# Performance work log

Hardware: AMD Instinct MI355X
Metric: run time of the kernel (lower is better)

## Reference

```python
import jax, jax.numpy as jnp
import numpy as np

B, S, T, D, V = 512, 128, 128, 512, 128  # batch, enc len, dec steps (=longest_smi), dim_model, output_size


def setup_inputs() -> dict:
    key = jax.random.key(0)
    ks = jax.random.split(key, 17)
    sc = 0.05
    return {
        "e_all": jax.random.normal(ks[0], (B, S, D), jnp.float32),
        "e_h": jax.random.normal(ks[1], (1, B, D), jnp.float32),
        "e_c": jax.random.normal(ks[2], (1, B, D), jnp.float32),
        "target": jax.random.randint(ks[3], (B, T), 0, T),
        # params (Linear weights stored [in, out], y = x @ W + b)
        "E": jax.random.normal(ks[4], (T, D), jnp.float32) * sc,        # Embedding(longest_smi, D)
        "Wa": jax.random.normal(ks[5], (D, D), jnp.float32) * sc,
        "ba": jnp.zeros((D,), jnp.float32),
        "Ua": jax.random.normal(ks[6], (D, D), jnp.float32) * sc,
        "bu": jnp.zeros((D,), jnp.float32),
        "Va": jax.random.normal(ks[7], (D, 1), jnp.float32) * sc,
        "bv": jnp.zeros((1,), jnp.float32),
        "W_ih": jax.random.normal(ks[8], (2 * D, 4 * D), jnp.float32) * sc,
        "b_ih": jnp.zeros((4 * D,), jnp.float32),
        "W_hh": jax.random.normal(ks[9], (D, 4 * D), jnp.float32) * sc,
        "b_hh": jnp.zeros((4 * D,), jnp.float32),
        "W_out": jax.random.normal(ks[10], (D, V), jnp.float32) * sc,
        "b_out": jnp.zeros((V,), jnp.float32),
    }


def reference(e_all, e_h, e_c, target, E, Wa, ba, Ua, bu, Va, bv,
              W_ih, b_ih, W_hh, b_hh, W_out, b_out):
    Bb = e_all.shape[0]
    # teacher forcing: step 0 input is token 0 (SOS), then target[:, :-1]
    idx = jnp.concatenate([jnp.zeros((Bb, 1), target.dtype), target[:, :-1]], axis=1)  # [B,T]
    emb_all = E[idx]                       # [B,T,D] (dropout is identity in eval)
    keys_proj = e_all @ Ua + bu            # Ua(keys), loop-invariant  [B,S,D]
    h0, c0 = e_h[0], e_c[0]                # [B,D]

    def step(carry, emb):
        h, c = carry
        q = (h + c) @ Wa + ba                                   # [B,D]  Wa(query)
        s = jnp.tanh(q[:, None, :] + keys_proj) @ Va + bv       # [B,S,1]
        w = jax.nn.softmax(s[..., 0], axis=-1)                  # [B,S]
        ctx = jnp.einsum('bs,bsd->bd', w, e_all)                # [B,D]
        x = jnp.concatenate([emb, ctx], axis=-1)                # [B,2D]
        g = x @ W_ih + b_ih + h @ W_hh + b_hh                   # [B,4D], torch gate order i,f,g,o
        i_, f_, g_, o_ = jnp.split(g, 4, axis=-1)
        c2 = jax.nn.sigmoid(f_) * c + jax.nn.sigmoid(i_) * jnp.tanh(g_)
        h2 = jax.nn.sigmoid(o_) * jnp.tanh(c2)
        out = h2 @ W_out + b_out                                # [B,V]
        return (h2, c2), (out, w)

    _, (outs, attns) = jax.lax.scan(step, (h0, c0), jnp.swapaxes(emb_all, 0, 1))
    outputs = jax.nn.log_softmax(jnp.swapaxes(outs, 0, 1), axis=-1)  # [B,T,V]
    cross_attn = jnp.swapaxes(attns, 0, 1)                           # [B,T,S]
    return outputs, cross_attn
```

## Files before the change

kernel.cpp:

```cpp
#include <hip/hip_runtime.h>

#define B_ 512
#define S_ 128
#define T_ 128
#define D_ 512
#define V_ 128
#define LDW 72

typedef __attribute__((ext_vector_type(8))) short s16x8;
typedef __attribute__((ext_vector_type(4))) short s16x4;
typedef __attribute__((ext_vector_type(4))) float f32x4;

__device__ __forceinline__ float b2f(unsigned short h) {
    union { unsigned int u; float f; } x; x.u = ((unsigned int)h) << 16; return x.f;
}
__device__ __forceinline__ unsigned short f2b(float f) {
    union { float f; unsigned int u; } x; x.f = f;
    unsigned int u = x.u; u += 0x7FFFu + ((u >> 16) & 1u);
    return (unsigned short)(u >> 16);
}
#if __has_builtin(__builtin_amdgcn_rcpf)
__device__ __forceinline__ float rcp_f(float x) { return __builtin_amdgcn_rcpf(x); }
#else
__device__ __forceinline__ float rcp_f(float x) { return 1.0f / x; }
#endif
__device__ __forceinline__ float sigm(float x) { return rcp_f(1.0f + __expf(-x)); }
__device__ __forceinline__ float tanh_fast(float x) {
    float e = __expf(2.0f * fabsf(x));
    float r = 1.0f - 2.0f * rcp_f(e + 1.0f);
    return copysignf(r, x);
}

#if __has_builtin(__builtin_amdgcn_cvt_f32_fp8)
__device__ __forceinline__ f32x4 fp8x4_dec(unsigned w) {
    f32x4 r;
    r[0] = __builtin_amdgcn_cvt_f32_fp8(w, 0);
    r[1] = __builtin_amdgcn_cvt_f32_fp8(w, 1);
    r[2] = __builtin_amdgcn_cvt_f32_fp8(w, 2);
    r[3] = __builtin_amdgcn_cvt_f32_fp8(w, 3);
    return r;
}
#else
__device__ __forceinline__ float fp8_dec_sw(unsigned w, int j) {
    unsigned char v = (w >> (8 * j)) & 0xFF;
    unsigned s = v >> 7, e = (v >> 3) & 0xF, m = v & 7;
    float r = (e == 0) ? ldexpf((float)m, -9) : ldexpf((float)(8 + m), (int)e - 10);
    return s ? -r : r;
}
__device__ __forceinline__ f32x4 fp8x4_dec(unsigned w) {
    f32x4 r;
    r[0] = fp8_dec_sw(w, 0); r[1] = fp8_dec_sw(w, 1);
    r[2] = fp8_dec_sw(w, 2); r[3] = fp8_dec_sw(w, 3);
    return r;
}
#endif

#if __has_builtin(__builtin_amdgcn_cvt_pk_fp8_f32)
__device__ __forceinline__ unsigned pk_fp8(float a, float b, float c, float d) {
    int r = 0;
    r = __builtin_amdgcn_cvt_pk_fp8_f32(a, b, r, false);
    r = __builtin_amdgcn_cvt_pk_fp8_f32(c, d, r, true);
    return (unsigned)r;
}
#else
__device__ __forceinline__ unsigned char f32_to_fp8_sw(float x) {
    unsigned s = x < 0.f ? 0x80u : 0u; float a = fabsf(x);
    if (a != a) return (unsigned char)(s | 0x7F);
    if (a >= 448.f) return (unsigned char)(s | 0x7E);
    if (a < 0.001953125f) { int m = (int)rintf(a * 512.0f); return (unsigned char)(s | (m > 7 ? 0x08 : m)); }
    int e; float fr = frexpf(a, &e);
    int m = (int)rintf(fr * 16.0f - 8.0f);
    int ee = e - 1 + 7;
    if (m == 8) { m = 0; ee += 1; }
    if (ee <= 0) { int mm = (int)rintf(a * 512.f); return (unsigned char)(s | (mm > 7 ? 0x08 : mm)); }
    if (ee >= 16) return (unsigned char)(s | 0x7E);
    return (unsigned char)(s | (ee << 3) | m);
}
__device__ __forceinline__ unsigned pk_fp8(float a, float b, float c, float d) {
    return (unsigned)f32_to_fp8_sw(a) | ((unsigned)f32_to_fp8_sw(b) << 8)
         | ((unsigned)f32_to_fp8_sw(c) << 16) | ((unsigned)f32_to_fp8_sw(d) << 24);
}
#endif

struct P {
    const int* target;
    const float* E; const float* bv; const float* ba; const float* bout;
    const short* vab;
    const unsigned char* ea8; const unsigned char* kp8;
    const short* WaT; const short* WehT; const short* WctxT; const short* WoutT;
    const float* bcat;
    short* qbf; short* xeh; short* ctxb; short* gpb;
    short* hcbf; short* h2bf; float* cst;
    float* out_logits; float* out_attn;
};

struct AttnS { float scp[4][64]; float wbuf[S_]; float cpart[4][D_]; };
struct OutS  { short As[64][LDW]; short Bs[128][LDW]; };
struct PG2   { short As[128][LDW]; short Bs[64][LDW]; };
struct GateS { short As[64][LDW]; short Bs[64][LDW]; float gt[64][65]; };
union SharedA { AttnS a; OutS o; };
union SharedC { OutS o; PG2 g; };

__device__ __forceinline__ void attn_phase(const P& p, AttnS& sh, int b, int step)
{
    const int t = threadIdx.x, lane = t & 63, wave = t >> 6;
    {
        const int sg = wave & 1, dh = wave >> 1;
        const int s = sg * 64 + lane;
        const unsigned char* kb = p.kp8 + (size_t)b * (S_ * D_);
        const short* qv = p.qbf + (size_t)b * D_;
        float acc = 0.f;
        #pragma unroll 4
        for (int i = 0; i < 16; ++i) {
            int g = dh * 16 + i;
            uint4 kw = *(const uint4*)(kb + ((size_t)g * 128 + s) * 16);
            const short* qg = qv + g * 16;
            const short* vg = p.vab + g * 16;
            s16x8 q0 = *(const s16x8*)(qg), q1 = *(const s16x8*)(qg + 8);
            s16x8 v0 = *(const s16x8*)(vg), v1 = *(const s16x8*)(vg + 8);
            f32x4 ka = fp8x4_dec(kw.x), kb4 = fp8x4_dec(kw.y);
            f32x4 kc = fp8x4_dec(kw.z), kd = fp8x4_dec(kw.w);
            #pragma unroll
            for (int j = 0; j < 4; ++j) {
                acc += tanh_fast(b2f((unsigned short)q0[j])     + ka[j])  * b2f((unsigned short)v0[j]);
                acc += tanh_fast(b2f((unsigned short)q0[4 + j]) + kb4[j]) * b2f((unsigned short)v0[4 + j]);
                acc += tanh_fast(b2f((unsigned short)q1[j])     + kc[j])  * b2f((unsigned short)v1[j]);
                acc += tanh_fast(b2f((unsigned short)q1[4 + j]) + kd[j])  * b2f((unsigned short)v1[4 + j]);
            }
        }
        sh.scp[wave][lane] = acc;
    }
    __syncthreads();
    if (wave == 0) {
        const float bvv = p.bv[0];
        float v0 = sh.scp[0][lane] + sh.scp[2][lane] + bvv;
        float v1 = sh.scp[1][lane] + sh.scp[3][lane] + bvv;
        float m = fmaxf(v0, v1);
        #pragma unroll
        for (int o = 32; o >= 1; o >>= 1) m = fmaxf(m, __shfl_xor(m, o));
        float e0 = __expf(v0 - m), e1 = __expf(v1 - m);
        float su = e0 + e1;
        #pragma unroll
        for (int o = 32; o >= 1; o >>= 1) su += __shfl_xor(su, o);
        float inv = rcp_f(su);
        float w0 = e0 * inv, w1 = e1 * inv;
        sh.wbuf[lane] = w0; sh.wbuf[lane + 64] = w1;
        float* ao = p.out_attn + ((size_t)b * T_ + step) * S_;
        ao[lane] = w0; ao[lane + 64] = w1;
    }
    __syncthreads();
    {
        const int d0 = lane * 8;
        f32x4 aA = {0.f,0.f,0.f,0.f}, aB = {0.f,0.f,0.f,0.f};
        const unsigned char* eb = p.ea8 + (size_t)b * S_ * D_ + d0;
        #pragma unroll 4
        for (int i = 0; i < 32; ++i) {
            int s = wave * 32 + i;
            float wv = sh.wbuf[s];
            uint2 ev = *(const uint2*)(eb + (size_t)s * D_);
            f32x4 ex = fp8x4_dec(ev.x), ey = fp8x4_dec(ev.y);
            #pragma unroll
            for (int j = 0; j < 4; ++j) aA[j] += wv * ex[j];
            #pragma unroll
            for (int j = 0; j < 4; ++j) aB[j] += wv * ey[j];
        }
        *(f32x4*)&sh.cpart[wave][d0]     = aA;
        *(f32x4*)&sh.cpart[wave][d0 + 4] = aB;
    }
    __syncthreads();
    {
        int dd = t * 2;
        float v0 = sh.cpart[0][dd]   + sh.cpart[1][dd]   + sh.cpart[2][dd]   + sh.cpart[3][dd];
        float v1 = sh.cpart[0][dd+1] + sh.cpart[1][dd+1] + sh.cpart[2][dd+1] + sh.cpart[3][dd+1];
        short2 o2; o2.x = (short)f2b(v0); o2.y = (short)f2b(v1);
        *(short2*)(p.ctxb + (size_t)b * D_ + dd) = o2;
    }
}

__device__ __forceinline__ void pgate_phase(const P& p, PG2& sh, int bid2)
{
    const int t = threadIdx.x, lane = t & 63, wave = t >> 6;
    const int lrow = lane & 15, kq = lane >> 4;
    const int m0 = (bid2 >> 5) * 128, n0 = (bid2 & 31) * 64;
    const int K = 1024;
    f32x4 acc[2][4] = {};
    for (int k0 = 0; k0 < K; k0 += 64) {
        s16x8 va[4], vb[2];
        #pragma unroll
        for (int r = 0; r < 4; ++r) {
            int idx = r * 256 + t, row = idx >> 3, seg = idx & 7;
            va[r] = *(const s16x8*)(p.xeh + (size_t)(m0 + row) * K + k0 + seg * 8);
        }
        #pragma unroll
        for (int r = 0; r < 2; ++r) {
            int idx = r * 256 + t, row = idx >> 3, seg = idx & 7;
            vb[r] = *(const s16x8*)(p.WehT + (size_t)(n0 + row) * K + k0 + seg * 8);
        }
        __syncthreads();
        #pragma unroll
        for (int r = 0; r < 4; ++r) {
            int idx = r * 256 + t, row = idx >> 3, seg = idx & 7;
            *(s16x8*)(&sh.As[row][seg * 8]) = va[r];
        }
        #pragma unroll
        for (int r = 0; r < 2; ++r) {
            int idx = r * 256 + t, row = idx >> 3, seg = idx & 7;
            *(s16x8*)(&sh.Bs[row][seg * 8]) = vb[r];
        }
        __syncthreads();
        #pragma unroll
        for (int kk = 0; kk < 64; kk += 32) {
            s16x8 af[2], bf[4];
            af[0] = *(const s16x8*)(&sh.As[wave * 32 + lrow][kk + kq * 8]);
            af[1] = *(const s16x8*)(&sh.As[wave * 32 + 16 + lrow][kk + kq * 8]);
            #pragma unroll
            for (int f = 0; f < 4; ++f)
                bf[f] = *(const s16x8*)(&sh.Bs[f * 16 + lrow][kk + kq * 8]);
            #pragma unroll
            for (int m2 = 0; m2 < 2; ++m2)
                #pragma unroll
                for (int n2 = 0; n2 < 4; ++n2)
                    acc[m2][n2] = __builtin_amdgcn_mfma_f32_16x16x32_bf16(af[m2], bf[n2], acc[m2][n2], 0, 0, 0);
        }
    }
    #pragma unroll
    for (int m2 = 0; m2 < 2; ++m2)
        #pragma unroll
        for (int n2 = 0; n2 < 4; ++n2) {
            int col = n0 + n2 * 16 + lrow;
            float bvv = p.bcat[col];
            #pragma unroll
            for (int j = 0; j < 4; ++j) {
                int row = m0 + wave * 32 + m2 * 16 + kq * 4 + j;
                p.gpb[(size_t)row * 2048 + col] = (short)f2b(acc[m2][n2][j] + bvv);
            }
        }
}

__device__ __forceinline__ void fgate_phase(const P& p, GateS& sh, int bid, int step)
{
    const int t = threadIdx.x, lane = t & 63, wave = t >> 6;
    const int wr = wave >> 1, wc = wave & 1;
    const int lrow = lane & 15, kq = lane >> 4;
    const int srow = t >> 3, sseg = t & 7;
    const int m0 = (bid >> 5) * 64, n0 = (bid & 31) * 64;
    f32x4 acc[2][2] = {};
    for (int k0 = 0; k0 < 512; k0 += 64) {
        s16x8 va0 = *(const s16x8*)(p.ctxb + (size_t)(m0 + srow) * 512 + k0 + sseg * 8);
        s16x8 va1 = *(const s16x8*)(p.ctxb + (size_t)(m0 + srow + 32) * 512 + k0 + sseg * 8);
        s16x8 vb0 = *(const s16x8*)(p.WctxT + (size_t)(n0 + srow) * 512 + k0 + sseg * 8);
        s16x8 vb1 = *(const s16x8*)(p.WctxT + (size_t)(n0 + srow + 32) * 512 + k0 + sseg * 8);
        __syncthreads();
        *(s16x8*)(&sh.As[srow][sseg * 8]) = va0;
        *(s16x8*)(&sh.As[srow + 32][sseg * 8]) = va1;
        *(s16x8*)(&sh.Bs[srow][sseg * 8]) = vb0;
        *(s16x8*)(&sh.Bs[srow + 32][sseg * 8]) = vb1;
        __syncthreads();
        #pragma unroll
        for (int kk = 0; kk < 64; kk += 32) {
            s16x8 af0 = *(const s16x8*)(&sh.As[wr * 32 + lrow][kk + kq * 8]);
            s16x8 af1 = *(const s16x8*)(&sh.As[wr * 32 + 16 + lrow][kk + kq * 8]);
            s16x8 bf0 = *(const s16x8*)(&sh.Bs[wc * 32 + lrow][kk + kq * 8]);
            s16x8 bf1 = *(const s16x8*)(&sh.Bs[wc * 32 + 16 + lrow][kk + kq * 8]);
            acc[0][0] = __builtin_amdgcn_mfma_f32_16x16x32_bf16(af0, bf0, acc[0][0], 0, 0, 0);
            acc[0][1] = __builtin_amdgcn_mfma_f32_16x16x32_bf16(af0, bf1, acc[0][1], 0, 0, 0);
            acc[1][0] = __builtin_amdgcn_mfma_f32_16x16x32_bf16(af1, bf0, acc[1][0], 0, 0, 0);
            acc[1][1] = __builtin_amdgcn_mfma_f32_16x16x32_bf16(af1, bf1, acc[1][1], 0, 0, 0);
        }
    }
    #pragma unroll
    for (int m2 = 0; m2 < 2; ++m2)
        #pragma unroll
        for (int n2 = 0; n2 < 2; ++n2) {
            int cl = wc * 32 + n2 * 16 + lrow;
            #pragma unroll
            for (int j = 0; j < 4; ++j) {
                int rl = wr * 32 + m2 * 16 + kq * 4 + j;
                sh.gt[rl][cl] = acc[m2][n2][j]
                              + b2f((unsigned short)p.gpb[(size_t)(m0 + rl) * 2048 + n0 + cl]);
            }
        }
    __syncthreads();
    const int rl4 = t >> 4, dl = t & 15;
    #pragma unroll
    for (int pass = 0; pass < 4; ++pass) {
        int row = pass * 16 + rl4;
        int b = m0 + row;
        int d = (n0 >> 2) + dl;
        float gi = sh.gt[row][dl * 4 + 0];
        float gf = sh.gt[row][dl * 4 + 1];
        float gg = sh.gt[row][dl * 4 + 2];
        float go = sh.gt[row][dl * 4 + 3];
        float cv = p.cst[(size_t)b * D_ + d];
        float c2 = sigm(gf) * cv + sigm(gi) * tanh_fast(gg);
        float h2 = sigm(go) * tanh_fast(c2);
        p.cst[(size_t)b * D_ + d] = c2;
        p.hcbf[(size_t)b * D_ + d] = (short)f2b(h2 + c2);
        p.h2bf[(size_t)b * D_ + d] = (short)f2b(h2);
        p.xeh[(size_t)b * 1024 + 512 + d] = (short)f2b(h2);
        int tok = p.target[b * T_ + step];
        p.xeh[(size_t)b * 1024 + d] = (short)f2b(p.E[(size_t)tok * D_ + d]);
    }
}

__device__ __forceinline__ void q_phase(const P& p, OutS& sh, int bid)
{
    const int t = threadIdx.x, lane = t & 63, wave = t >> 6;
    const int lrow = lane & 15, kq = lane >> 4;
    const int srow = t >> 3, sseg = t & 7;
    const int m0 = (bid >> 4) * 64, n0 = (bid & 15) * 32;
    f32x4 acc0 = {}, acc1 = {};
    for (int k0 = 0; k0 < 512; k0 += 64) {
        s16x8 va0 = *(const s16x8*)(p.hcbf + (size_t)(m0 + srow) * 512 + k0 + sseg * 8);
        s16x8 va1 = *(const s16x8*)(p.hcbf + (size_t)(m0 + srow + 32) * 512 + k0 + sseg * 8);
        int brow = n0 + (srow & 31);
        s16x8 vb0 = *(const s16x8*)(p.WaT + (size_t)brow * 512 + k0 + sseg * 8);
        __syncthreads();
        *(s16x8*)(&sh.As[srow][sseg * 8]) = va0;
        *(s16x8*)(&sh.As[srow + 32][sseg * 8]) = va1;
        if (srow < 32) *(s16x8*)(&sh.Bs[srow][sseg * 8]) = vb0;
        __syncthreads();
        #pragma unroll
        for (int kk = 0; kk < 64; kk += 32) {
            s16x8 af  = *(const s16x8*)(&sh.As[wave * 16 + lrow][kk + kq * 8]);
            s16x8 bf0 = *(const s16x8*)(&sh.Bs[lrow][kk + kq * 8]);
            s16x8 bf1 = *(const s16x8*)(&sh.Bs[16 + lrow][kk + kq * 8]);
            acc0 = __builtin_amdgcn_mfma_f32_16x16x32_bf16(af, bf0, acc0, 0, 0, 0);
            acc1 = __builtin_amdgcn_mfma_f32_16x16x32_bf16(af, bf1, acc1, 0, 0, 0);
        }
    }
    #pragma unroll
    for (int n2 = 0; n2 < 2; ++n2) {
        int col = n0 + n2 * 16 + lrow;
        float bvv = p.ba[col];
        f32x4 av = n2 ? acc1 : acc0;
        #pragma unroll
        for (int j = 0; j < 4; ++j) {
            int row = m0 + wave * 16 + kq * 4 + j;
            p.qbf[(size_t)row * 512 + col] = (short)f2b(av[j] + bvv);
        }
    }
}

__device__ __forceinline__ void out_phase(const P& p, OutS& sh, int obid, int step)
{
    const int t = threadIdx.x, lane = t & 63, wave = t >> 6;
    const int lrow = lane & 15, kq = lane >> 4;
    const int srow = t >> 3, sseg = t & 7;
    const int m0 = obid * 64;
    f32x4 acc[8] = {};
    for (int k0 = 0; k0 < 512; k0 += 64) {
        s16x8 va0 = *(const s16x8*)(p.h2bf + (size_t)(m0 + srow) * 512 + k0 + sseg * 8);
        s16x8 va1 = *(const s16x8*)(p.h2bf + (size_t)(m0 + srow + 32) * 512 + k0 + sseg * 8);
        s16x8 vb[4];
        #pragma unroll
        for (int p4 = 0; p4 < 4; ++p4)
            vb[p4] = *(const s16x8*)(p.WoutT + (size_t)(srow + p4 * 32) * 512 + k0 + sseg * 8);
        __syncthreads();
        *(s16x8*)(&sh.As[srow][sseg * 8]) = va0;
        *(s16x8*)(&sh.As[srow + 32][sseg * 8]) = va1;
        #pragma unroll
        for (int p4 = 0; p4 < 4; ++p4) *(s16x8*)(&sh.Bs[srow + p4 * 32][sseg * 8]) = vb[p4];
        __syncthreads();
        #pragma unroll
        for (int kk = 0; kk < 64; kk += 32) {
            s16x8 a = *(const s16x8*)(&sh.As[wave * 16 + lrow][kk + kq * 8]);
            #pragma unroll
            for (int f = 0; f < 8; ++f) {
                s16x8 b = *(const s16x8*)(&sh.Bs[f * 16 + lrow][kk + kq * 8]);
                acc[f] = __builtin_amdgcn_mfma_f32_16x16x32_bf16(a, b, acc[f], 0, 0, 0);
            }
        }
    }
    float colb[8];
    #pragma unroll
    for (int f = 0; f < 8; ++f) colb[f] = p.bout[f * 16 + lrow];
    #pragma unroll
    for (int j = 0; j < 4; ++j) {
        float v[8]; float mx = -1e30f;
        #pragma unroll
        for (int f = 0; f < 8; ++f) { v[f] = acc[f][j] + colb[f]; mx = fmaxf(mx, v[f]); }
        #pragma unroll
        for (int o = 1; o < 16; o <<= 1) mx = fmaxf(mx, __shfl_xor(mx, o));
        float sum = 0.f;
        #pragma unroll
        for (int f = 0; f < 8; ++f) sum += __expf(v[f] - mx);
        #pragma unroll
        for (int o = 1; o < 16; o <<= 1) sum += __shfl_xor(sum, o);
        float lse = mx + __logf(sum);
        int row = m0 + wave * 16 + kq * 4 + j;
        float* orow = p.out_logits + ((size_t)row * T_ + step) * V_;
        #pragma unroll
        for (int f = 0; f < 8; ++f) orow[f * 16 + lrow] = v[f] - lse;
    }
}

__global__ __launch_bounds__(256, 2) void kA(P p, int step) {
    __shared__ SharedA sh;
    const int bid = blockIdx.x;
    if (bid < 512)     attn_phase(p, sh.a, bid, step);
    else if (step > 0) out_phase(p, sh.o, bid - 512, step - 1);
}
__global__ __launch_bounds__(256, 2) void kB(P p, int step) {
    __shared__ GateS sh;
    fgate_phase(p, sh, blockIdx.x, step);
}
__global__ __launch_bounds__(256, 2) void kC(P p) {
    __shared__ SharedC sh;
    const int bid = blockIdx.x;
    if (bid < 128) q_phase(p, sh.o, bid);
    else           pgate_phase(p, sh.g, bid - 128);
}
__global__ __launch_bounds__(256, 2) void kOutLast(P p, int step) {
    __shared__ OutS sh;
    out_phase(p, sh, blockIdx.x, step);
}

__global__ __launch_bounds__(256)
void gemm64(const short* __restrict__ A, const short* __restrict__ Bt,
            const float* __restrict__ bias, short* __restrict__ Cp,
            int M, int N, int K)
{
    __shared__ __align__(16) short As[64][LDW];
    __shared__ __align__(16) short Bs[64][LDW];
    const int t = threadIdx.x;
    const int lane = t & 63, wave = t >> 6;
    const int wr = wave >> 1, wc = wave & 1;
    const int lrow = lane & 15, kq = lane >> 4;
    const int m0 = blockIdx.y * 64, n0 = blockIdx.x * 64;
    const int srow = t >> 3, sseg = t & 7;
    f32x4 acc[2][2] = {};
    for (int k0 = 0; k0 < K; k0 += 64) {
        s16x8 va0 = *(const s16x8*)(A + (size_t)(m0 + srow) * K + k0 + sseg * 8);
        s16x8 va1 = *(const s16x8*)(A + (size_t)(m0 + srow + 32) * K + k0 + sseg * 8);
        s16x8 vb0 = *(const s16x8*)(Bt + (size_t)(n0 + srow) * K + k0 + sseg * 8);
        s16x8 vb1 = *(const s16x8*)(Bt + (size_t)(n0 + srow + 32) * K + k0 + sseg * 8);
        __syncthreads();
        *(s16x8*)(&As[srow][sseg * 8]) = va0;
        *(s16x8*)(&As[srow + 32][sseg * 8]) = va1;
        *(s16x8*)(&Bs[srow][sseg * 8]) = vb0;
        *(s16x8*)(&Bs[srow + 32][sseg * 8]) = vb1;
        __syncthreads();
        for (int kk = 0; kk < 64; kk += 32) {
            s16x8 af[2], bf[2];
            af[0] = *(const s16x8*)(&As[wr * 32 + lrow][kk + kq * 8]);
            af[1] = *(const s16x8*)(&As[wr * 32 + 16 + lrow][kk + kq * 8]);
            bf[0] = *(const s16x8*)(&Bs[wc * 32 + lrow][kk + kq * 8]);
            bf[1] = *(const s16x8*)(&Bs[wc * 32 + 16 + lrow][kk + kq * 8]);
            for (int m2 = 0; m2 < 2; ++m2)
                for (int n2 = 0; n2 < 2; ++n2)
                    acc[m2][n2] = __builtin_amdgcn_mfma_f32_16x16x32_bf16(af[m2], bf[n2], acc[m2][n2], 0, 0, 0);
        }
    }
    for (int m2 = 0; m2 < 2; ++m2)
        for (int n2 = 0; n2 < 2; ++n2) {
            int col = n0 + wc * 32 + n2 * 16 + lrow;
            float bvv = bias ? bias[col] : 0.0f;
            for (int j = 0; j < 4; ++j) {
                int row = m0 + wr * 32 + m2 * 16 + kq * 4 + j;
                Cp[(size_t)row * N + col] = (short)f2b(acc[m2][n2][j] + bvv);
            }
        }
}

__global__ __launch_bounds__(256)
void transpose_kp8(const short* __restrict__ in, unsigned char* __restrict__ out)
{
    const int b = blockIdx.x, t = threadIdx.x;
    const size_t ibase = (size_t)b * (S_ * D_);
    for (int k = t; k < 32 * S_; k += 256) {
        int g = k >> 7, s = k & 127;
        const short* src = in + ibase + (size_t)s * D_ + g * 16;
        unsigned w[4];
        #pragma unroll
        for (int q4 = 0; q4 < 4; ++q4) {
            w[q4] = pk_fp8(b2f((unsigned short)src[q4 * 4 + 0]), b2f((unsigned short)src[q4 * 4 + 1]),
                           b2f((unsigned short)src[q4 * 4 + 2]), b2f((unsigned short)src[q4 * 4 + 3]));
        }
        uint4 o; o.x = w[0]; o.y = w[1]; o.z = w[2]; o.w = w[3];
        *(uint4*)(out + ibase + ((size_t)g * S_ + s) * 16) = o;
    }
}

__global__ __launch_bounds__(256)
void cast_fp8_v4(const float* __restrict__ in, unsigned char* __restrict__ out, int n4)
{
    int i = blockIdx.x * 256 + threadIdx.x;
    int stride = gridDim.x * 256;
    for (; i < n4; i += stride) {
        f32x4 v = ((const f32x4*)in)[i];
        ((unsigned*)out)[i] = pk_fp8(v[0], v[1], v[2], v[3]);
    }
}

__global__ __launch_bounds__(256)
void init_state(const float* __restrict__ e_h, const float* __restrict__ e_c,
                float* __restrict__ c, short* __restrict__ hcbf,
                short* __restrict__ xeh, const float* __restrict__ E)
{
    int gid = blockIdx.x * 256 + threadIdx.x;
    int b = gid >> 9, d = gid & 511;
    float h0 = e_h[gid], c0 = e_c[gid];
    c[gid] = c0;
    hcbf[gid] = (short)f2b(h0 + c0);
    xeh[(size_t)b * 1024 + 512 + d] = (short)f2b(h0);
    xeh[(size_t)b * 1024 + d] = (short)f2b(E[d]);
}

__global__ __launch_bounds__(256)
void transpose_cast(const float* __restrict__ in, short* __restrict__ out,
                    int N, int ostride, int koff, int gate_perm)
{
    __shared__ float tile[64][65];
    int t = threadIdx.x;
    int n0 = blockIdx.x * 64, k0 = blockIdx.y * 64;
    int cc = t & 63, r4 = t >> 6;
    for (int i = 0; i < 16; ++i) {
        int r = i * 4 + r4;
        tile[r][cc] = in[(size_t)(k0 + r) * N + n0 + cc];
    }
    __syncthreads();
    for (int i = 0; i < 16; ++i) {
        int nr = i * 4 + r4;
        int ng = n0 + nr;
        int np = gate_perm ? ((ng & 511) * 4 + (ng >> 9)) : ng;
        out[(size_t)np * ostride + koff + k0 + cc] = (short)f2b(tile[cc][nr]);
    }
}

__global__ __launch_bounds__(256)
void cast_bf16_v4(const float* __restrict__ in, short* __restrict__ out, int n4)
{
    int i = blockIdx.x * 256 + threadIdx.x;
    int stride = gridDim.x * 256;
    for (; i < n4; i += stride) {
        f32x4 v = ((const f32x4*)in)[i];
        s16x4 o;
        for (int j = 0; j < 4; ++j) o[j] = (short)f2b(v[j]);
        ((s16x4*)out)[i] = o;
    }
}

__global__ __launch_bounds__(256)
void make_bcat(const float* __restrict__ b_ih, const float* __restrict__ b_hh, float* __restrict__ bcat)
{
    int i = blockIdx.x * 256 + threadIdx.x;
    if (i < 2048) {
        int np = (i & 511) * 4 + (i >> 9);
        bcat[np] = b_ih[i] + b_hh[i];
    }
}

extern "C" void kernel_launch(void* const* d_in, const int* in_sizes, int n_in,
                              void* d_out, int out_size, void* d_ws, size_t ws_size,
                              hipStream_t stream)
{
    const float* e_all  = (const float*)d_in[0];
    const float* e_h    = (const float*)d_in[1];
    const float* e_c    = (const float*)d_in[2];
    const int*   target = (const int*)d_in[3];
    const float* E      = (const float*)d_in[4];
    const float* Wa     = (const float*)d_in[5];
    const float* ba     = (const float*)d_in[6];
    const float* Ua     = (const float*)d_in[7];
    const float* bu     = (const float*)d_in[8];
    const float* Va     = (const float*)d_in[9];
    const float* bv     = (const float*)d_in[10];
    const float* W_ih   = (const float*)d_in[11];
    const float* b_ih   = (const float*)d_in[12];
    const float* W_hh   = (const float*)d_in[13];
    const float* b_hh   = (const float*)d_in[14];
    const float* W_out  = (const float*)d_in[15];
    const float* b_out  = (const float*)d_in[16];

    char* ws = (char*)d_ws;
    size_t off = 0;
    auto alloc = [&](size_t bytes) { void* p = ws + off; off += (bytes + 255) & ~255ull; return p; };
    short* ealb  = (short*)alloc((size_t)B_ * S_ * D_ * 2);
    short* kpb   = (short*)alloc((size_t)B_ * S_ * D_ * 2);
    unsigned char* kp8 = (unsigned char*)alloc((size_t)B_ * S_ * D_);
    unsigned char* ea8 = (unsigned char*)alloc((size_t)B_ * S_ * D_);
    short* WaT   = (short*)alloc((size_t)D_ * D_ * 2);
    short* UaT   = (short*)alloc((size_t)D_ * D_ * 2);
    short* WehT  = (short*)alloc((size_t)2048 * 1024 * 2);
    short* WctxT = (short*)alloc((size_t)2048 * 512 * 2);
    short* WoutT = (short*)alloc((size_t)V_ * D_ * 2);
    float* bcat  = (float*)alloc(2048 * 4);
    short* qbf   = (short*)alloc((size_t)B_ * D_ * 2);
    short* vab   = (short*)alloc((size_t)D_ * 2);
    short* xeh   = (short*)alloc((size_t)B_ * 1024 * 2);
    short* ctxb  = (short*)alloc((size_t)B_ * D_ * 2);
    short* gpb   = (short*)alloc((size_t)B_ * 2048 * 2);
    short* hcbf  = (short*)alloc((size_t)B_ * D_ * 2);
    short* h2bf  = (short*)alloc((size_t)B_ * D_ * 2);
    float* cst   = (float*)alloc((size_t)B_ * D_ * 4);
    if (off > ws_size) return;

    float* out_logits = (float*)d_out;
    float* out_attn   = (float*)d_out + (size_t)B_ * T_ * V_;

    cast_bf16_v4<<<4096, 256, 0, stream>>>(e_all, ealb, B_ * S_ * D_ / 4);
    cast_fp8_v4<<<4096, 256, 0, stream>>>(e_all, ea8, B_ * S_ * D_ / 4);
    cast_bf16_v4<<<1,    256, 0, stream>>>(Va, vab, D_ / 4);
    transpose_cast<<<dim3(8, 8),  256, 0, stream>>>(Wa,  WaT,  512,  512, 0, 0);
    transpose_cast<<<dim3(8, 8),  256, 0, stream>>>(Ua,  UaT,  512,  512, 0, 0);
    transpose_cast<<<dim3(32, 8), 256, 0, stream>>>(W_ih,              WehT,  2048, 1024, 0,   1);
    transpose_cast<<<dim3(32, 8), 256, 0, stream>>>(W_ih + 512 * 2048, WctxT, 2048, 512,  0,   1);
    transpose_cast<<<dim3(32, 8), 256, 0, stream>>>(W_hh,              WehT,  2048, 1024, 512, 1);
    transpose_cast<<<dim3(2, 8),  256, 0, stream>>>(W_out, WoutT, 128, 512, 0, 0);
    make_bcat<<<8, 256, 0, stream>>>(b_ih, b_hh, bcat);
    gemm64<<<dim3(8, 1024), 256, 0, stream>>>(ealb, UaT, bu, kpb, B_ * S_, 512, 512);
    transpose_kp8<<<512, 256, 0, stream>>>(kpb, kp8);
    init_state<<<1024, 256, 0, stream>>>(e_h, e_c, cst, hcbf, xeh, E);

    P pp;
    pp.target = target; pp.E = E; pp.bv = bv; pp.ba = ba; pp.bout = b_out;
    pp.vab = vab;
    pp.ea8 = ea8; pp.kp8 = kp8; pp.WaT = WaT; pp.WehT = WehT; pp.WctxT = WctxT; pp.WoutT = WoutT;
    pp.bcat = bcat; pp.qbf = qbf; pp.xeh = xeh; pp.ctxb = ctxb; pp.gpb = gpb;
    pp.hcbf = hcbf; pp.h2bf = h2bf; pp.cst = cst;
    pp.out_logits = out_logits; pp.out_attn = out_attn;

    kC<<<256, 256, 0, stream>>>(pp);

    for (int t = 0; t < T_; ++t) {
        kA<<<520, 256, 0, stream>>>(pp, t);
        kB<<<256, 256, 0, stream>>>(pp, t);
        kC<<<256, 256, 0, stream>>>(pp);
    }
    kOutLast<<<8, 256, 0, stream>>>(pp, T_ - 1);
    (void)n_in; (void)in_sizes; (void)out_size;
}
```

Measured before the change: 6.449 ms.

## Split gate pre-GEMM along K, move output projection into kC, use Pade tanh

The precomputed gate GEMM over [emb,h] (K=1024) is split into two K=512 halves computed by separate blocks into two buffers. The fused gate kernel sums both partials. This doubles the block count in kC and shortens each block's serial K loop. The output-projection blocks move from kA into kC, which drops the kOutLast launch. The attention score tanh becomes a clamped Pade rational approximation to avoid an exp per element, at some accuracy risk and with an extra buffer read in the gate kernel.

```diff
diff --git a/kernel.cpp b/kernel.cpp
--- a/kernel.cpp
+++ b/kernel.cpp
@@ -29,6 +29,13 @@
     float e = __expf(2.0f * fabsf(x));
     float r = 1.0f - 2.0f * rcp_f(e + 1.0f);
     return copysignf(r, x);
+}
+__device__ __forceinline__ float tanh_pade(float x) {
+    float t = x * x;
+    float num = x * fmaf(t, 105.0f + t, 945.0f);
+    float den = fmaf(t, fmaf(t, 15.0f, 420.0f), 945.0f);
+    float r = num * rcp_f(den);
+    return fminf(1.0f, fmaxf(-1.0f, r));
 }
 
 #if __has_builtin(__builtin_amdgcn_cvt_f32_fp8)
@@ -89,7 +96,7 @@
     const unsigned char* ea8; const unsigned char* kp8;
     const short* WaT; const short* WehT; const short* WctxT; const short* WoutT;
     const float* bcat;
-    short* qbf; short* xeh; short* ctxb; short* gpb;
+    short* qbf; short* xeh; short* ctxb; short* gpA; short* gpB;
     short* hcbf; short* h2bf; float* cst;
     float* out_logits; float* out_attn;
 };
@@ -98,7 +105,6 @@
 struct OutS  { short As[64][LDW]; short Bs[128][LDW]; };
 struct PG2   { short As[128][LDW]; short Bs[64][LDW]; };
 struct GateS { short As[64][LDW]; short Bs[64][LDW]; float gt[64][65]; };
-union SharedA { AttnS a; OutS o; };
 union SharedC { OutS o; PG2 g; };
 
 __device__ __forceinline__ void attn_phase(const P& p, AttnS& sh, int b, int step)
@@ -122,10 +128,10 @@
             f32x4 kc = fp8x4_dec(kw.z), kd = fp8x4_dec(kw.w);
             #pragma unroll
             for (int j = 0; j < 4; ++j) {
-                acc += tanh_fast(b2f((unsigned short)q0[j])     + ka[j])  * b2f((unsigned short)v0[j]);
-                acc += tanh_fast(b2f((unsigned short)q0[4 + j]) + kb4[j]) * b2f((unsigned short)v0[4 + j]);
-                acc += tanh_fast(b2f((unsigned short)q1[j])     + kc[j])  * b2f((unsigned short)v1[j]);
-                acc += tanh_fast(b2f((unsigned short)q1[4 + j]) + kd[j])  * b2f((unsigned short)v1[4 + j]);
+                acc += tanh_pade(b2f((unsigned short)q0[j])     + ka[j])  * b2f((unsigned short)v0[j]);
+                acc += tanh_pade(b2f((unsigned short)q0[4 + j]) + kb4[j]) * b2f((unsigned short)v0[4 + j]);
+                acc += tanh_pade(b2f((unsigned short)q1[j])     + kc[j])  * b2f((unsigned short)v1[j]);
+                acc += tanh_pade(b2f((unsigned short)q1[4 + j]) + kd[j])  * b2f((unsigned short)v1[4 + j]);
             }
         }
         sh.scp[wave][lane] = acc;
@@ -177,24 +183,24 @@
     }
 }
 
-__device__ __forceinline__ void pgate_phase(const P& p, PG2& sh, int bid2)
+__device__ __forceinline__ void pgate_phase(const P& p, PG2& sh, int bid2, int koff,
+                                            short* __restrict__ gpp, bool addb)
 {
     const int t = threadIdx.x, lane = t & 63, wave = t >> 6;
     const int lrow = lane & 15, kq = lane >> 4;
     const int m0 = (bid2 >> 5) * 128, n0 = (bid2 & 31) * 64;
-    const int K = 1024;
     f32x4 acc[2][4] = {};
-    for (int k0 = 0; k0 < K; k0 += 64) {
+    for (int k0 = 0; k0 < 512; k0 += 64) {
         s16x8 va[4], vb[2];
         #pragma unroll
         for (int r = 0; r < 4; ++r) {
             int idx = r * 256 + t, row = idx >> 3, seg = idx & 7;
-            va[r] = *(const s16x8*)(p.xeh + (size_t)(m0 + row) * K + k0 + seg * 8);
+            va[r] = *(const s16x8*)(p.xeh + (size_t)(m0 + row) * 1024 + koff + k0 + seg * 8);
         }
         #pragma unroll
         for (int r = 0; r < 2; ++r) {
             int idx = r * 256 + t, row = idx >> 3, seg = idx & 7;
-            vb[r] = *(const s16x8*)(p.WehT + (size_t)(n0 + row) * K + k0 + seg * 8);
+            vb[r] = *(const s16x8*)(p.WehT + (size_t)(n0 + row) * 1024 + koff + k0 + seg * 8);
         }
         __syncthreads();
         #pragma unroll
@@ -228,11 +234,11 @@
         #pragma unroll
         for (int n2 = 0; n2 < 4; ++n2) {
             int col = n0 + n2 * 16 + lrow;
-            float bvv = p.bcat[col];
+            float bvv = addb ? p.bcat[col] : 0.0f;
             #pragma unroll
             for (int j = 0; j < 4; ++j) {
                 int row = m0 + wave * 32 + m2 * 16 + kq * 4 + j;
-                p.gpb[(size_t)row * 2048 + col] = (short)f2b(acc[m2][n2][j] + bvv);
+                gpp[(size_t)row * 2048 + col] = (short)f2b(acc[m2][n2][j] + bvv);
             }
         }
 }
@@ -276,8 +282,10 @@
             #pragma unroll
             for (int j = 0; j < 4; ++j) {
                 int rl = wr * 32 + m2 * 16 + kq * 4 + j;
+                size_t gidx = (size_t)(m0 + rl) * 2048 + n0 + cl;
                 sh.gt[rl][cl] = acc[m2][n2][j]
-                              + b2f((unsigned short)p.gpb[(size_t)(m0 + rl) * 2048 + n0 + cl]);
+                              + b2f((unsigned short)p.gpA[gidx])
+                              + b2f((unsigned short)p.gpB[gidx]);
             }
         }
     __syncthreads();
@@ -396,24 +404,21 @@
 }
 
 __global__ __launch_bounds__(256, 2) void kA(P p, int step) {
-    __shared__ SharedA sh;
-    const int bid = blockIdx.x;
-    if (bid < 512)     attn_phase(p, sh.a, bid, step);
-    else if (step > 0) out_phase(p, sh.o, bid - 512, step - 1);
+    __shared__ AttnS sh;
+    attn_phase(p, sh, blockIdx.x, step);
 }
 __global__ __launch_bounds__(256, 2) void kB(P p, int step) {
     __shared__ GateS sh;
     fgate_phase(p, sh, blockIdx.x, step);
 }
-__global__ __launch_bounds__(256, 2) void kC(P p) {
+template<bool INIT>
+__global__ __launch_bounds__(256, 2) void kC(P p, int step) {
     __shared__ SharedC sh;
     const int bid = blockIdx.x;
-    if (bid < 128) q_phase(p, sh.o, bid);
-    else           pgate_phase(p, sh.g, bid - 128);
-}
-__global__ __launch_bounds__(256, 2) void kOutLast(P p, int step) {
-    __shared__ OutS sh;
-    out_phase(p, sh, blockIdx.x, step);
+    if (bid < 128)       q_phase(p, sh.o, bid);
+    else if (bid < 256)  pgate_phase(p, sh.g, bid - 128, 0,   p.gpA, true);
+    else if (bid < 384)  pgate_phase(p, sh.g, bid - 256, 512, p.gpB, false);
+    else if (!INIT)      out_phase(p, sh.o, bid - 384, step);
 }
 
 __global__ __launch_bounds__(256)
@@ -590,7 +595,8 @@
     short* vab   = (short*)alloc((size_t)D_ * 2);
     short* xeh   = (short*)alloc((size_t)B_ * 1024 * 2);
     short* ctxb  = (short*)alloc((size_t)B_ * D_ * 2);
-    short* gpb   = (short*)alloc((size_t)B_ * 2048 * 2);
+    short* gpA   = (short*)alloc((size_t)B_ * 2048 * 2);
+    short* gpB   = (short*)alloc((size_t)B_ * 2048 * 2);
     short* hcbf  = (short*)alloc((size_t)B_ * D_ * 2);
     short* h2bf  = (short*)alloc((size_t)B_ * D_ * 2);
     float* cst   = (float*)alloc((size_t)B_ * D_ * 4);
@@ -617,17 +623,16 @@
     pp.target = target; pp.E = E; pp.bv = bv; pp.ba = ba; pp.bout = b_out;
     pp.vab = vab;
     pp.ea8 = ea8; pp.kp8 = kp8; pp.WaT = WaT; pp.WehT = WehT; pp.WctxT = WctxT; pp.WoutT = WoutT;
-    pp.bcat = bcat; pp.qbf = qbf; pp.xeh = xeh; pp.ctxb = ctxb; pp.gpb = gpb;
+    pp.bcat = bcat; pp.qbf = qbf; pp.xeh = xeh; pp.ctxb = ctxb; pp.gpA = gpA; pp.gpB = gpB;
     pp.hcbf = hcbf; pp.h2bf = h2bf; pp.cst = cst;
     pp.out_logits = out_logits; pp.out_attn = out_attn;
 
-    kC<<<256, 256, 0, stream>>>(pp);
+    kC<true><<<384, 256, 0, stream>>>(pp, 0);
 
     for (int t = 0; t < T_; ++t) {
-        kA<<<520, 256, 0, stream>>>(pp, t);
+        kA<<<512, 256, 0, stream>>>(pp, t);
         kB<<<256, 256, 0, stream>>>(pp, t);
-        kC<<<256, 256, 0, stream>>>(pp);
-    }
-    kOutLast<<<8, 256, 0, stream>>>(pp, T_ - 1);
+        kC<false><<<392, 256, 0, stream>>>(pp, t);
+    }
     (void)n_in; (void)in_sizes; (void)out_size;
 }
```

Measured after the change: 6.259 ms. -3.0%, faster.
